# Kernel tuning notes

Hardware: AMD Instinct MI355X
Metric: run time of the kernel (lower is better)

## Reference

```python
import jax, jax.numpy as jnp
import numpy as np

D_MODEL = 1024
NUM_HEADS = 16
DEPTH = D_MODEL // NUM_HEADS
B, S = 2, 2048


def setup_inputs() -> dict:
    key = jax.random.key(0)
    ks = jax.random.split(key, 13)
    sc = 1.0 / np.sqrt(D_MODEL)
    inp = {
        "q": jax.random.normal(ks[0], (B, S, D_MODEL), jnp.float32),
        "k": jax.random.normal(ks[1], (B, S, D_MODEL), jnp.float32),
        "v": jax.random.normal(ks[2], (B, S, D_MODEL), jnp.float32),
        "mask": jax.random.randint(ks[3], (B, 1, S, S), 0, 2).astype(jnp.float32),
        "wq": jax.random.normal(ks[4], (D_MODEL, D_MODEL), jnp.float32) * sc,
        "bq": jnp.zeros((D_MODEL,), jnp.float32),
        "wk": jax.random.normal(ks[5], (D_MODEL, D_MODEL), jnp.float32) * sc,
        "bk": jnp.zeros((D_MODEL,), jnp.float32),
        "wv": jax.random.normal(ks[6], (D_MODEL, D_MODEL), jnp.float32) * sc,
        "bv": jnp.zeros((D_MODEL,), jnp.float32),
        "wo": jax.random.normal(ks[7], (D_MODEL, D_MODEL), jnp.float32) * sc,
        "bo": jnp.zeros((D_MODEL,), jnp.float32),
    }
    return inp


def _split_heads(x):
    # [B,S,D] -> [B,H,S,depth]
    b, s, _ = x.shape
    return x.reshape(b, s, NUM_HEADS, DEPTH).transpose(0, 2, 1, 3)


def reference(q, k, v, mask, wq, bq, wk, bk, wv, bv, wo, bo):
    qh = _split_heads(q @ wq.T + bq)
    kh = _split_heads(k @ wk.T + bk)
    vh = _split_heads(v @ wv.T + bv)
    logits = jnp.einsum("bhqd,bhkd->bhqk", qh, kh) / jnp.sqrt(
        jnp.asarray(DEPTH, jnp.float32))
    logits = logits + mask * (-1e9)
    attn = jax.nn.softmax(logits, axis=-1)
    out = jnp.einsum("bhqk,bhkd->bhqd", attn, vh)
    out = out.transpose(0, 2, 1, 3).reshape(q.shape[0], -1, D_MODEL)
    return out @ wo.T + bo
```

## Files before the change

kernel.cpp:

```cpp
#include <hip/hip_runtime.h>

#define D_MODEL 1024
#define NHEADS  16
#define DEPTH   64
#define BATCH   2
#define SEQ     2048
#define MROWS   (BATCH * SEQ)
#define QSCALE  0.125f

typedef unsigned short u16;
typedef unsigned int   u32;
typedef unsigned long long u64;
typedef __bf16 bf16x8 __attribute__((ext_vector_type(8)));
typedef float  f32x4  __attribute__((ext_vector_type(4)));

__device__ __forceinline__ u16 f2b(float f) {
    return __builtin_bit_cast(u16, static_cast<__bf16>(f));
}
__device__ __forceinline__ bf16x8 ldb8(const u16* p) {
    return __builtin_bit_cast(bf16x8, *(const uint4*)p);
}

__global__ __launch_bounds__(256) void pack_mask(
    const float* __restrict__ mask, u64* __restrict__ bits)
{
    const int w    = blockIdx.x * 4 + (threadIdx.x >> 6);
    const int lane = threadIdx.x & 63;
    float m = mask[(size_t)w * 64 + lane];
    u64 b = __ballot(m > 0.5f);
    if (lane == 0) bits[w] = b;
}

__global__ __launch_bounds__(256, 3) void proj3(
    const float* __restrict__ q, const float* __restrict__ k, const float* __restrict__ v,
    const float* __restrict__ wq, const float* __restrict__ wk, const float* __restrict__ wv,
    const float* __restrict__ bq, const float* __restrict__ bk, const float* __restrict__ bv,
    u16* __restrict__ qws, u16* __restrict__ kws, u16* __restrict__ vtws)
{
    __shared__ __align__(16) u16 ldsA[128 * 40];
    __shared__ __align__(16) u16 ldsB[128 * 40];

    const int z = blockIdx.z;
    const float* X  = (z == 0) ? q  : (z == 1) ? k  : v;
    const float* W  = (z == 0) ? wq : (z == 1) ? wk : wv;
    const float* Bi = (z == 0) ? bq : (z == 1) ? bk : bv;
    u16* dst        = (z == 0) ? qws : (z == 1) ? kws : vtws;

    const int tid  = threadIdx.x;
    const int wv_  = tid >> 6;
    const int lane = tid & 63;
    const int quad = lane >> 4;
    const int l15  = lane & 15;
    const int bx = blockIdx.y >> 2;
    const int by = (blockIdx.x << 2) | (blockIdx.y & 3);
    const int wm = (wv_ >> 1) * 64;
    const int wn = (wv_ & 1) * 64;

    f32x4 acc[4][4];
    for (int i = 0; i < 4; ++i)
        for (int j = 0; j < 4; ++j)
            acc[i][j] = (f32x4){0.f, 0.f, 0.f, 0.f};

    const int rowA0 = by * 128;
    const int rowB0 = bx * 128;

    const int sr = tid >> 3;
    const int sc = (tid & 7) * 4;

    float4 pa[4], pb[4];
    #pragma unroll
    for (int i = 0; i < 4; ++i) {
        pa[i] = *(const float4*)&X[(size_t)(rowA0 + sr + i * 32) * D_MODEL + sc];
        pb[i] = *(const float4*)&W[(size_t)(rowB0 + sr + i * 32) * D_MODEL + sc];
    }

    for (int it = 0; it < 32; ++it) {
        #pragma unroll
        for (int i = 0; i < 4; ++i) {
            ushort4 ha, hb;
            ha.x = f2b(pa[i].x); ha.y = f2b(pa[i].y); ha.z = f2b(pa[i].z); ha.w = f2b(pa[i].w);
            hb.x = f2b(pb[i].x); hb.y = f2b(pb[i].y); hb.z = f2b(pb[i].z); hb.w = f2b(pb[i].w);
            *(ushort4*)&ldsA[(sr + i * 32) * 40 + sc] = ha;
            *(ushort4*)&ldsB[(sr + i * 32) * 40 + sc] = hb;
        }
        __syncthreads();

        if (it < 31) {
            const int k0 = (it + 1) * 32;
            #pragma unroll
            for (int i = 0; i < 4; ++i) {
                pa[i] = *(const float4*)&X[(size_t)(rowA0 + sr + i * 32) * D_MODEL + k0 + sc];
                pb[i] = *(const float4*)&W[(size_t)(rowB0 + sr + i * 32) * D_MODEL + k0 + sc];
            }
        }

        bf16x8 af[4], bfr[4];
        #pragma unroll
        for (int t = 0; t < 4; ++t) {
            af[t]  = ldb8(&ldsA[(wm + t * 16 + l15) * 40 + quad * 8]);
            bfr[t] = ldb8(&ldsB[(wn + t * 16 + l15) * 40 + quad * 8]);
        }
        #pragma unroll
        for (int mt = 0; mt < 4; ++mt)
            #pragma unroll
            for (int nt = 0; nt < 4; ++nt)
                acc[mt][nt] = __builtin_amdgcn_mfma_f32_16x16x32_bf16(af[mt], bfr[nt], acc[mt][nt], 0, 0, 0);
        __syncthreads();
    }

    #pragma unroll
    for (int nt = 0; nt < 4; ++nt) {
        int n = bx * 128 + wn + nt * 16 + l15;
        float bvv = Bi[n];
        int h = n >> 6, d = n & 63;
        #pragma unroll
        for (int mt = 0; mt < 4; ++mt) {
            #pragma unroll
            for (int r = 0; r < 4; ++r) {
                int m = by * 128 + wm + mt * 16 + quad * 4 + r;
                float c = acc[mt][nt][r] + bvv;
                if (z == 0) c *= QSCALE;
                int b = m >> 11, s = m & (SEQ - 1);
                if (z != 2)
                    dst[(((size_t)(b * NHEADS + h) * SEQ) + s) * DEPTH + d] = f2b(c);
                else
                    dst[(((size_t)(b * NHEADS + h) * DEPTH) + d) * SEQ + s] = f2b(c);
            }
        }
    }
}

__global__ __launch_bounds__(256) void gemm_out(
    const u16* __restrict__ X, const float* __restrict__ W,
    const float* __restrict__ bias, float* __restrict__ out)
{
    __shared__ __align__(16) u16 ldsA[128 * 40];
    __shared__ __align__(16) u16 ldsB[64 * 40];

    const int tid  = threadIdx.x;
    const int wv_  = tid >> 6;
    const int lane = tid & 63;
    const int quad = lane >> 4;
    const int l15  = lane & 15;
    const int bx = ((blockIdx.y >> 2) << 1) | (blockIdx.x >> 3);
    const int by = ((blockIdx.x & 7) << 2) | (blockIdx.y & 3);
    const int wm = (wv_ >> 1) * 64;
    const int wn = (wv_ & 1) * 32;

    f32x4 acc[4][2];
    for (int i = 0; i < 4; ++i)
        for (int j = 0; j < 2; ++j)
            acc[i][j] = (f32x4){0.f, 0.f, 0.f, 0.f};

    const int rowA0 = by * 128;
    const int rowB0 = bx * 64;

    const int ar = tid >> 2, akc = (tid & 3) * 8;
    const int br = tid >> 3, bc = (tid & 7) * 4;

    uint4  paA[2];
    float4 paB[2];
    #pragma unroll
    for (int i = 0; i < 2; ++i) {
        paA[i] = *(const uint4*)&X[(size_t)(rowA0 + ar + i * 64) * D_MODEL + akc];
        paB[i] = *(const float4*)&W[(size_t)(rowB0 + br + i * 32) * D_MODEL + bc];
    }

    for (int it = 0; it < 32; ++it) {
        #pragma unroll
        for (int i = 0; i < 2; ++i) {
            *(uint4*)&ldsA[(ar + i * 64) * 40 + akc] = paA[i];
            ushort4 hb;
            hb.x = f2b(paB[i].x); hb.y = f2b(paB[i].y); hb.z = f2b(paB[i].z); hb.w = f2b(paB[i].w);
            *(ushort4*)&ldsB[(br + i * 32) * 40 + bc] = hb;
        }
        __syncthreads();

        if (it < 31) {
            const int k0 = (it + 1) * 32;
            #pragma unroll
            for (int i = 0; i < 2; ++i) {
                paA[i] = *(const uint4*)&X[(size_t)(rowA0 + ar + i * 64) * D_MODEL + k0 + akc];
                paB[i] = *(const float4*)&W[(size_t)(rowB0 + br + i * 32) * D_MODEL + k0 + bc];
            }
        }

        bf16x8 af[4], bfr[2];
        #pragma unroll
        for (int t = 0; t < 4; ++t)
            af[t] = ldb8(&ldsA[(wm + t * 16 + l15) * 40 + quad * 8]);
        #pragma unroll
        for (int t = 0; t < 2; ++t)
            bfr[t] = ldb8(&ldsB[(wn + t * 16 + l15) * 40 + quad * 8]);
        #pragma unroll
        for (int mt = 0; mt < 4; ++mt)
            #pragma unroll
            for (int nt = 0; nt < 2; ++nt)
                acc[mt][nt] = __builtin_amdgcn_mfma_f32_16x16x32_bf16(af[mt], bfr[nt], acc[mt][nt], 0, 0, 0);
        __syncthreads();
    }

    #pragma unroll
    for (int nt = 0; nt < 2; ++nt) {
        int n = bx * 64 + wn + nt * 16 + l15;
        float bvv = bias[n];
        #pragma unroll
        for (int mt = 0; mt < 4; ++mt) {
            #pragma unroll
            for (int r = 0; r < 4; ++r) {
                int m = by * 128 + wm + mt * 16 + quad * 4 + r;
                out[(size_t)m * D_MODEL + n] = acc[mt][nt][r] + bvv;
            }
        }
    }
}

__global__ __launch_bounds__(256, 3) void flash_attn(
    const u16* __restrict__ Q, const u16* __restrict__ K,
    const u16* __restrict__ Vt, const u64* __restrict__ maskbits,
    u16* __restrict__ O)
{
    __shared__ __align__(16) u16 ldsK[2][64 * 64];
    __shared__ __align__(16) u16 ldsV[2][64 * 64];
    __shared__ __align__(16) u16 ldsP[4][16 * 72];

    const int tid  = threadIdx.x;
    const int wv_  = tid >> 6;
    const int lane = tid & 63;
    const int quad = lane >> 4;
    const int l15  = lane & 15;
    const int bh = ((blockIdx.x & 7) << 2) | (blockIdx.y & 3);
    const int qt = ((blockIdx.y >> 2) << 2) | (blockIdx.x >> 3);
    const int b  = bh >> 4, h = bh & 15;
    const int q0 = qt * 64 + wv_ * 16;

    const u16* Qb = Q  + (size_t)bh * SEQ * DEPTH;
    const u16* Kb = K  + (size_t)bh * SEQ * DEPTH;
    const u16* Vb = Vt + (size_t)bh * DEPTH * SEQ;
    const u64* MB = maskbits + (size_t)b * SEQ * (SEQ / 64);

    const int srow = tid >> 3;
    const int sc8  = tid & 7;
    const int swz  = ((sc8 ^ (srow & 7)) * 8);
    const int kdst0 = srow * 64 + swz;
    const int kdst1 = (srow + 32) * 64 + swz;

    const int xk0 = ((quad ^ (l15 & 7)) * 8);
    const int xk1 = (((4 + quad) ^ (l15 & 7)) * 8);

    bf16x8 aq0 = ldb8(&Qb[(q0 + l15) * DEPTH + quad * 8]);
    bf16x8 aq1 = ldb8(&Qb[(q0 + l15) * DEPTH + 32 + quad * 8]);

    f32x4 oa[4];
    for (int i = 0; i < 4; ++i) oa[i] = (f32x4){0.f, 0.f, 0.f, 0.f};
    float lrow[4] = {0.f, 0.f, 0.f, 0.f};

    u16* myP = ldsP[wv_];

    uint4 kreg0 = *(const uint4*)&Kb[(size_t)srow * DEPTH + sc8 * 8];
    uint4 kreg1 = *(const uint4*)&Kb[(size_t)(srow + 32) * DEPTH + sc8 * 8];
    uint4 vreg0 = *(const uint4*)&Vb[(size_t)srow * SEQ + sc8 * 8];
    uint4 vreg1 = *(const uint4*)&Vb[(size_t)(srow + 32) * SEQ + sc8 * 8];

    for (int it = 0; it < 32; ++it) {
        const int buf = it & 1;
        u16* Kl = ldsK[buf];
        u16* Vl = ldsV[buf];

        *(uint4*)&Kl[kdst0] = kreg0;
        *(uint4*)&Kl[kdst1] = kreg1;
        *(uint4*)&Vl[kdst0] = vreg0;
        *(uint4*)&Vl[kdst1] = vreg1;
        __syncthreads();

        if (it < 31) {
            const int kb2 = (it + 1) * 64;
            kreg0 = *(const uint4*)&Kb[(size_t)(kb2 + srow) * DEPTH + sc8 * 8];
            kreg1 = *(const uint4*)&Kb[(size_t)(kb2 + srow + 32) * DEPTH + sc8 * 8];
            vreg0 = *(const uint4*)&Vb[(size_t)srow * SEQ + kb2 + sc8 * 8];
            vreg1 = *(const uint4*)&Vb[(size_t)(srow + 32) * SEQ + kb2 + sc8 * 8];
        }

        u32 tlo[4], thi[4];
        #pragma unroll
        for (int r = 0; r < 4; ++r) {
            u64 t = MB[(size_t)(q0 + quad * 4 + r) * (SEQ / 64) + it] >> l15;
            tlo[r] = (u32)t;
            thi[r] = (u32)(t >> 32);
        }

        #pragma unroll
        for (int cc = 0; cc < 4; ++cc) {
            const int row = cc * 16 + l15;
            bf16x8 bk0 = ldb8(&Kl[row * 64 + xk0]);
            bf16x8 bk1 = ldb8(&Kl[row * 64 + xk1]);
            f32x4 z = (f32x4){0.f, 0.f, 0.f, 0.f};
            z = __builtin_amdgcn_mfma_f32_16x16x32_bf16(aq0, bk0, z, 0, 0, 0);
            z = __builtin_amdgcn_mfma_f32_16x16x32_bf16(aq1, bk1, z, 0, 0, 0);
            #pragma unroll
            for (int r = 0; r < 4; ++r) {
                u32 w   = (cc < 2) ? tlo[r] : thi[r];
                u32 bit = (cc & 1) ? ((w >> 16) & 1u) : (w & 1u);
                float e = __expf(z[r]);
                float p = bit ? 0.f : e;
                lrow[r] += p;
                myP[(quad * 4 + r) * 72 + cc * 16 + l15] = f2b(p);
            }
        }

        __builtin_amdgcn_wave_barrier();
        __builtin_amdgcn_s_waitcnt(0xc07f);
        __builtin_amdgcn_wave_barrier();
        bf16x8 pa0 = ldb8(&myP[l15 * 72 + quad * 8]);
        bf16x8 pa1 = ldb8(&myP[l15 * 72 + 32 + quad * 8]);

        #pragma unroll
        for (int n = 0; n < 4; ++n) {
            const int row = n * 16 + l15;
            bf16x8 bv0 = ldb8(&Vl[row * 64 + xk0]);
            bf16x8 bv1 = ldb8(&Vl[row * 64 + xk1]);
            oa[n] = __builtin_amdgcn_mfma_f32_16x16x32_bf16(pa0, bv0, oa[n], 0, 0, 0);
            oa[n] = __builtin_amdgcn_mfma_f32_16x16x32_bf16(pa1, bv1, oa[n], 0, 0, 0);
        }
    }

    #pragma unroll
    for (int r = 0; r < 4; ++r) {
        float s = lrow[r];
        #pragma unroll
        for (int off = 1; off < 16; off <<= 1)
            s += __shfl_xor(s, off, 64);
        lrow[r] = 1.0f / s;
    }
    #pragma unroll
    for (int n = 0; n < 4; ++n)
        #pragma unroll
        for (int r = 0; r < 4; ++r) {
            int m = q0 + quad * 4 + r;
            O[((size_t)b * SEQ + m) * D_MODEL + h * DEPTH + n * 16 + l15] =
                f2b(oa[n][r] * lrow[r]);
        }
}

extern "C" void kernel_launch(void* const* d_in, const int* in_sizes, int n_in,
                              void* d_out, int out_size, void* d_ws, size_t ws_size,
                              hipStream_t stream) {
    const float* q    = (const float*)d_in[0];
    const float* k    = (const float*)d_in[1];
    const float* v    = (const float*)d_in[2];
    const float* mask = (const float*)d_in[3];
    const float* wq   = (const float*)d_in[4];
    const float* bq   = (const float*)d_in[5];
    const float* wk   = (const float*)d_in[6];
    const float* bk   = (const float*)d_in[7];
    const float* wv   = (const float*)d_in[8];
    const float* bv   = (const float*)d_in[9];
    const float* wo   = (const float*)d_in[10];
    const float* bo   = (const float*)d_in[11];

    u16* base = (u16*)d_ws;
    const size_t seg = (size_t)BATCH * NHEADS * SEQ * DEPTH;
    u16* qws  = base;
    u16* kws  = base + seg;
    u16* vtws = base + 2 * seg;
    u16* ows  = base + 3 * seg;
    u64* mbits = (u64*)(base + 4 * seg);

    dim3 blk(256);
    hipLaunchKernelGGL(pack_mask, dim3(BATCH * SEQ * (SEQ / 64) / 4), blk, 0, stream, mask, mbits);

    dim3 gp(D_MODEL / 128, MROWS / 128, 3);
    hipLaunchKernelGGL(proj3, gp, blk, 0, stream,
                       q, k, v, wq, wk, wv, bq, bk, bv, qws, kws, vtws);

    dim3 ga(SEQ / 64, BATCH * NHEADS);
    hipLaunchKernelGGL(flash_attn, ga, blk, 0, stream, qws, kws, vtws, mbits, ows);

    dim3 go(D_MODEL / 64, MROWS / 128);
    hipLaunchKernelGGL(gemm_out, go, blk, 0, stream, ows, wo, bo, (float*)d_out);
}
```

Baseline: 324.9 us.

## Use exp2 with folded log2e scale, MFMA row sums, swizzled P buffer

Folds log2(e) into the Q scale so the softmax exponent uses the native exp2 instruction instead of __expf. The per-lane row-sum accumulation and final cross-lane shuffle reduction are replaced by an MFMA of P against a ones vector. The P staging buffer in LDS is changed from padded stride-72 rows to XOR-swizzled stride-64 rows. Occupancy is raised via launch_bounds from 3 to 4 blocks. The row sum is now computed from the bf16-rounded P, which slightly changes numerics, and the extra MFMAs add some matrix-core work.

```diff
diff --git a/kernel.cpp b/kernel.cpp
--- a/kernel.cpp
+++ b/kernel.cpp
@@ -6,13 +6,19 @@
 #define BATCH   2
 #define SEQ     2048
 #define MROWS   (BATCH * SEQ)
-#define QSCALE  0.125f
+#define QSCALE  0.18033688011112042f
 
 typedef unsigned short u16;
 typedef unsigned int   u32;
 typedef unsigned long long u64;
 typedef __bf16 bf16x8 __attribute__((ext_vector_type(8)));
 typedef float  f32x4  __attribute__((ext_vector_type(4)));
+
+#if __has_builtin(__builtin_amdgcn_exp2f)
+#define EXP2(x) __builtin_amdgcn_exp2f(x)
+#else
+#define EXP2(x) exp2f(x)
+#endif
 
 __device__ __forceinline__ u16 f2b(float f) {
     return __builtin_bit_cast(u16, static_cast<__bf16>(f));
@@ -215,14 +221,14 @@
     }
 }
 
-__global__ __launch_bounds__(256, 3) void flash_attn(
+__global__ __launch_bounds__(256, 4) void flash_attn(
     const u16* __restrict__ Q, const u16* __restrict__ K,
     const u16* __restrict__ Vt, const u64* __restrict__ maskbits,
     u16* __restrict__ O)
 {
     __shared__ __align__(16) u16 ldsK[2][64 * 64];
     __shared__ __align__(16) u16 ldsV[2][64 * 64];
-    __shared__ __align__(16) u16 ldsP[4][16 * 72];
+    __shared__ __align__(16) u16 ldsP[4][16 * 64];
 
     const int tid  = threadIdx.x;
     const int wv_  = tid >> 6;
@@ -251,11 +257,27 @@
     bf16x8 aq0 = ldb8(&Qb[(q0 + l15) * DEPTH + quad * 8]);
     bf16x8 aq1 = ldb8(&Qb[(q0 + l15) * DEPTH + 32 + quad * 8]);
 
+    bf16x8 vones;
+    #pragma unroll
+    for (int i = 0; i < 8; ++i) vones[i] = (__bf16)1.0f;
+
     f32x4 oa[4];
     for (int i = 0; i < 4; ++i) oa[i] = (f32x4){0.f, 0.f, 0.f, 0.f};
-    float lrow[4] = {0.f, 0.f, 0.f, 0.f};
+    f32x4 lacc = (f32x4){0.f, 0.f, 0.f, 0.f};
 
     u16* myP = ldsP[wv_];
+
+    int wp[4][4];
+    #pragma unroll
+    for (int cc = 0; cc < 4; ++cc)
+        #pragma unroll
+        for (int r = 0; r < 4; ++r) {
+            const int row  = quad * 4 + r;
+            const int colg = cc * 2 + (l15 >> 3);
+            wp[cc][r] = row * 64 + ((colg ^ (row & 7)) * 8) + (l15 & 7);
+        }
+    const int rp0 = l15 * 64 + ((quad ^ (l15 & 7)) * 8);
+    const int rp1 = l15 * 64 + (((4 + quad) ^ (l15 & 7)) * 8);
 
     uint4 kreg0 = *(const uint4*)&Kb[(size_t)srow * DEPTH + sc8 * 8];
     uint4 kreg1 = *(const uint4*)&Kb[(size_t)(srow + 32) * DEPTH + sc8 * 8];
@@ -301,18 +323,20 @@
             for (int r = 0; r < 4; ++r) {
                 u32 w   = (cc < 2) ? tlo[r] : thi[r];
                 u32 bit = (cc & 1) ? ((w >> 16) & 1u) : (w & 1u);
-                float e = __expf(z[r]);
+                float e = EXP2(z[r]);
                 float p = bit ? 0.f : e;
-                lrow[r] += p;
-                myP[(quad * 4 + r) * 72 + cc * 16 + l15] = f2b(p);
+                myP[wp[cc][r]] = f2b(p);
             }
         }
 
         __builtin_amdgcn_wave_barrier();
         __builtin_amdgcn_s_waitcnt(0xc07f);
         __builtin_amdgcn_wave_barrier();
-        bf16x8 pa0 = ldb8(&myP[l15 * 72 + quad * 8]);
-        bf16x8 pa1 = ldb8(&myP[l15 * 72 + 32 + quad * 8]);
+        bf16x8 pa0 = ldb8(&myP[rp0]);
+        bf16x8 pa1 = ldb8(&myP[rp1]);
+
+        lacc = __builtin_amdgcn_mfma_f32_16x16x32_bf16(pa0, vones, lacc, 0, 0, 0);
+        lacc = __builtin_amdgcn_mfma_f32_16x16x32_bf16(pa1, vones, lacc, 0, 0, 0);
 
         #pragma unroll
         for (int n = 0; n < 4; ++n) {
@@ -324,21 +348,18 @@
         }
     }
 
-    #pragma unroll
-    for (int r = 0; r < 4; ++r) {
-        float s = lrow[r];
-        #pragma unroll
-        for (int off = 1; off < 16; off <<= 1)
-            s += __shfl_xor(s, off, 64);
-        lrow[r] = 1.0f / s;
-    }
+    float inv[4];
+    #pragma unroll
+    for (int r = 0; r < 4; ++r)
+        inv[r] = 1.0f / lacc[r];
+
     #pragma unroll
     for (int n = 0; n < 4; ++n)
         #pragma unroll
         for (int r = 0; r < 4; ++r) {
             int m = q0 + quad * 4 + r;
             O[((size_t)b * SEQ + m) * D_MODEL + h * DEPTH + n * 16 + l15] =
-                f2b(oa[n][r] * lrow[r]);
+                f2b(oa[n][r] * inv[r]);
         }
 }
 
```

New measurement: 317.5 us. 2.3% less time.
